# Optimization experiments

Measured on AMD Instinct MI355X. Metric: run time of the kernel, lower is better.

The kernel has to match this reference:

```python
import jax, jax.numpy as jnp
import numpy as np

B, C, D, H, W = 4, 320, 16, 16, 16
E, DK, DV = 2, 32, 160  # heads, key dim, value dim
EPS = 1e-6


def setup_inputs() -> dict:
    key = jax.random.key(0)
    ks = jax.random.split(key, 8)
    s_in = 1.0 / np.sqrt(C)
    s_mg = 1.0 / np.sqrt(E * DV)
    return {
        "x": jax.random.normal(ks[0], (B, C, D, H, W), jnp.float32),
        # pointwise (1x1x1) conv weights, stacked over heads
        "Wq": jax.random.normal(ks[1], (E, DK, C), jnp.float32) * s_in,
        "bq": jax.random.normal(ks[2], (E, DK), jnp.float32) * 0.01,
        "Wk": jax.random.normal(ks[3], (E, DK, C), jnp.float32) * s_in,
        "bk": jax.random.normal(ks[4], (E, DK), jnp.float32) * 0.01,
        "Wv": jax.random.normal(ks[5], (E, DV, C), jnp.float32) * s_in,
        "bv": jax.random.normal(ks[6], (E, DV), jnp.float32) * 0.01,
        # merging 1x1x1 conv: dv*num_heads -> C
        "Wm": jax.random.normal(ks[7], (C, E * DV), jnp.float32) * s_mg,
        "bm": jnp.zeros((C,), jnp.float32),
    }


def reference(x, Wq, bq, Wk, bk, Wv, bv, Wm, bm):
    b, c = x.shape[0], x.shape[1]
    xf = x.reshape(b, c, -1)  # [B, C, N], N = prod(spatial)

    def proj(Wt, bt):
        # 1x1x1 conv over all heads at once: [B, E, d, N]
        return jnp.einsum('ekc,bcn->bekn', Wt, xf) + bt[None, :, :, None]

    Q = proj(Wq, bq)
    K = proj(Wk, bk)
    V = proj(Wv, bv)  # [B, E, DV, N]

    def l2norm(t):
        # F.normalize over channel dim (dim=1 of [B, dk, N] per head)
        n = jnp.linalg.norm(t, axis=2, keepdims=True)
        return t / jnp.maximum(n, EPS)

    Qn = l2norm(Q)
    Kn = l2norm(K)

    # spatial attention: contract over key channels -> [B, E, N, N]
    A = jax.nn.softmax(jnp.einsum('bekn,bekm->benm', Qn, Kn), axis=-1)
    R = jnp.einsum('benm,bevm->bevn', A, V)  # [B, E, DV, N]

    # concat heads along channel dim, then merge conv + residual
    Rcat = R.reshape(b, E * DV, -1)  # [B, E*DV, N]
    out = jnp.einsum('cf,bfn->bcn', Wm, Rcat) + bm[None, :, None]
    return out.reshape(x.shape) + x
```

## Files before the change

### kernel.cpp

```cpp
#include <hip/hip_runtime.h>
#include <hip/hip_bf16.h>

#define BN 4
#define CN 320
#define NN 4096
#define EN 2
#define DKN 32
#define DVN 160

typedef __bf16 bf16;
typedef __bf16 bf16x8 __attribute__((ext_vector_type(8)));
typedef float f32x4 __attribute__((ext_vector_type(4)));

static __device__ __forceinline__ f32x4 mfma16(bf16x8 a, bf16x8 b, f32x4 c) {
  return __builtin_amdgcn_mfma_f32_16x16x32_bf16(a, b, c, 0, 0, 0);
}


__global__ __launch_bounds__(256) void k_prep(
    const float* __restrict__ Wq, const float* __restrict__ bq,
    const float* __restrict__ Wk, const float* __restrict__ bk,
    const float* __restrict__ Wv, const float* __restrict__ bv,
    const float* __restrict__ Wm,
    bf16* __restrict__ W_all, bf16* __restrict__ Wm_bf, float* __restrict__ b_all) {
  int t = blockIdx.x * 256 + threadIdx.x;
  if (t < 448 * CN) {
    int r = t / CN;
    float v;
    if (r < 64) v = Wq[t];
    else if (r < 128) v = Wk[t - 64 * CN];
    else v = Wv[t - 128 * CN];
    W_all[t] = (bf16)v;
  }
  if (t < 320 * 320) Wm_bf[t] = (bf16)Wm[t];
  if (t < 448) {
    float v;
    if (t < 64) v = bq[t];
    else if (t < 128) v = bk[t - 64];
    else v = bv[t - 128];
    b_all[t] = v;
  }
}

__global__ __launch_bounds__(256) void k_xt(const float* __restrict__ x, bf16* __restrict__ xT) {
  int blk = blockIdx.x;
  int b = blk / 640;
  int rem = blk - b * 640;
  int cc = rem >> 4;
  int nb = rem & 15;
  int n = nb * 256 + threadIdx.x;
  const float* xp = x + ((size_t)b * CN + cc * 8) * NN + n;
  bf16x8 v;
#pragma unroll
  for (int j = 0; j < 8; j++) v[j] = (bf16)xp[(size_t)j * NN];
  *(bf16x8*)(xT + ((size_t)b * NN + n) * CN + cc * 8) = v;
}

__global__ __launch_bounds__(256) void k_proj(
    const bf16* __restrict__ W_all, const float* __restrict__ b_all,
    const bf16* __restrict__ xT, float* __restrict__ QK, bf16* __restrict__ Vc) {
  int blk = blockIdx.x;
  int b = blk / 448;
  int rem = blk - b * 448;
  int mt = rem >> 4, nb = rem & 15;
  int w = threadIdx.x >> 6, l = threadIdx.x & 63;
  int lg = l >> 4, lr = l & 15;
  int m0 = mt * 16;
  int n0 = nb * 256 + w * 64;
  f32x4 acc[4] = {};
  const bf16* wp = W_all + (m0 + lr) * CN + 8 * lg;
  const bf16* xp = xT + ((size_t)b * NN + n0 + lr) * CN + 8 * lg;
#pragma unroll 2
  for (int c0 = 0; c0 < CN; c0 += 32) {
    bf16x8 a = *(const bf16x8*)(wp + c0);
#pragma unroll
    for (int j = 0; j < 4; j++) {
      bf16x8 bb = *(const bf16x8*)(xp + j * 16 * CN + c0);
      acc[j] = mfma16(a, bb, acc[j]);
    }
  }
#pragma unroll
  for (int i = 0; i < 4; i++) {
    int row = m0 + 4 * lg + i;
    float bias = b_all[row];
    if (row < 128) {
      float* qk = QK + ((size_t)b * 128 + row) * NN + n0 + lr;
#pragma unroll
      for (int j = 0; j < 4; j++) qk[j * 16] = acc[j][i] + bias;
    } else {
      int rr = row - 128;
      int e = rr / 160, dvl = rr - e * 160;
      int vt = dvl >> 4, lrc = dvl & 15;
      size_t beI = (size_t)(b * 2 + e);
#pragma unroll
      for (int j = 0; j < 4; j++) {
        int key = n0 + j * 16 + lr;
        int T = key >> 5, h = (key >> 4) & 1, g = (key >> 2) & 3, ic = key & 3;
        Vc[(((beI * 128 + T) * 10 + vt) * 4 + g) * 128 + lrc * 8 + h * 4 + ic] =
            (bf16)(acc[j][i] + bias);
      }
    }
  }
}

__global__ __launch_bounds__(256) void k_norm(
    const float* __restrict__ QK, bf16* __restrict__ Qn, bf16* __restrict__ Kn) {
  int t = blockIdx.x * 256 + threadIdx.x;
  int isk = t >> 15;
  int r = t & 32767;
  int b = r >> 13, e = (r >> 12) & 1, n = r & (NN - 1);
  const float* p = QK + ((size_t)b * 128 + isk * 64 + e * 32) * NN + n;
  float v[32];
  float ss = 0.f;
#pragma unroll
  for (int d = 0; d < 32; d++) { float q = p[(size_t)d * NN]; v[d] = q; ss += q * q; }
  float s = 1.0f / fmaxf(sqrtf(ss), 1e-6f);
  bf16* o = (isk ? Kn : Qn) + ((size_t)(b * 2 + e) * NN + n) * 32;
#pragma unroll
  for (int d0 = 0; d0 < 32; d0 += 8) {
    bf16x8 vo;
#pragma unroll
    for (int j = 0; j < 8; j++) vo[j] = (bf16)(v[d0 + j] * s);
    *(bf16x8*)(o + d0) = vo;
  }
}

__global__ __launch_bounds__(256) void k_attn(
    const bf16* __restrict__ Qn, const bf16* __restrict__ Kn,
    const bf16* __restrict__ Vc, bf16* __restrict__ Rt) {
  __shared__ float sbuf[64][83];
  int blk = blockIdx.x;
  int be = blk & 7, qc = blk >> 3;
  int w = threadIdx.x >> 6, l = threadIdx.x & 63;
  int lg = l >> 4, lr = l & 15;
  int qb = qc * 32;
  const bf16* qbase = Qn + ((size_t)be * NN + qb) * 32 + 8 * lg;
  bf16x8 qf0 = *(const bf16x8*)(qbase + lr * 32);
  bf16x8 qf1 = *(const bf16x8*)(qbase + (16 + lr) * 32);
  const bf16* kbase = Kn + (size_t)be * NN * 32 + 8 * lg;
  const bf16* vbase = Vc + (size_t)be * (128 * 10 * 512) + (size_t)l * 8;
  int mstart = w * (NN / 4), mend = mstart + (NN / 4);
  f32x4 acc0[10] = {};
  f32x4 acc1[10] = {};
  float rs0 = 0.f, rs1 = 0.f;
  bf16x8 kf0 = *(const bf16x8*)(kbase + (size_t)(mstart + lr) * 32);
  bf16x8 kf1 = *(const bf16x8*)(kbase + (size_t)(mstart + 16 + lr) * 32);
  for (int m0 = mstart; m0 < mend; m0 += 32) {
    const bf16* vp = vbase + (size_t)(m0 >> 5) * (10 * 512);
    bf16x8 vf[10];
#pragma unroll
    for (int vt = 0; vt < 10; vt++) vf[vt] = *(const bf16x8*)(vp + vt * 512);
    f32x4 zero = {};
    f32x4 s00 = mfma16(kf0, qf0, zero);
    f32x4 s01 = mfma16(kf1, qf0, zero);
    f32x4 s10 = mfma16(kf0, qf1, zero);
    f32x4 s11 = mfma16(kf1, qf1, zero);
    if (m0 + 32 < mend) {
      kf0 = *(const bf16x8*)(kbase + (size_t)(m0 + 32 + lr) * 32);
      kf1 = *(const bf16x8*)(kbase + (size_t)(m0 + 48 + lr) * 32);
    }
    bf16x8 pf0, pf1;
#pragma unroll
    for (int i = 0; i < 4; i++) {
      float e00 = __expf(s00[i]), e01 = __expf(s01[i]);
      float e10 = __expf(s10[i]), e11 = __expf(s11[i]);
      rs0 += e00 + e01;
      rs1 += e10 + e11;
      pf0[i] = (bf16)e00; pf0[4 + i] = (bf16)e01;
      pf1[i] = (bf16)e10; pf1[4 + i] = (bf16)e11;
    }
    __builtin_amdgcn_s_setprio(1);
#pragma unroll
    for (int vt = 0; vt < 10; vt++) {
      acc0[vt] = mfma16(pf0, vf[vt], acc0[vt]);
      acc1[vt] = mfma16(pf1, vf[vt], acc1[vt]);
    }
    __builtin_amdgcn_s_setprio(0);
  }
  for (int r = 1; r < 4; ++r) {
    if (w == r) {
      float* p = &sbuf[l][0];
#pragma unroll
      for (int vt = 0; vt < 10; vt++)
#pragma unroll
        for (int i = 0; i < 4; i++) {
          p[vt * 4 + i] = acc0[vt][i];
          p[40 + vt * 4 + i] = acc1[vt][i];
        }
      p[80] = rs0; p[81] = rs1;
    }
    __syncthreads();
    if (w == 0) {
      const float* p = &sbuf[l][0];
#pragma unroll
      for (int vt = 0; vt < 10; vt++)
#pragma unroll
        for (int i = 0; i < 4; i++) {
          acc0[vt][i] += p[vt * 4 + i];
          acc1[vt][i] += p[40 + vt * 4 + i];
        }
      rs0 += p[80]; rs1 += p[81];
    }
    __syncthreads();
  }
  if (w == 0) {
    rs0 += __shfl_xor(rs0, 16); rs0 += __shfl_xor(rs0, 32);
    rs1 += __shfl_xor(rs1, 16); rs1 += __shfl_xor(rs1, 32);
    f32x4 rinv0, rinv1;
#pragma unroll
    for (int i = 0; i < 4; i++) {
      rinv0[i] = 1.0f / __shfl(rs0, 4 * lg + i);
      rinv1[i] = 1.0f / __shfl(rs1, 4 * lg + i);
    }
    int b = be >> 1, e = be & 1;
#pragma unroll
    for (int vt = 0; vt < 10; vt++) {
#pragma unroll
      for (int i = 0; i < 4; i++) {
        int q0 = qb + 4 * lg + i;
        int q1 = qb + 16 + 4 * lg + i;
        Rt[((size_t)b * NN + q0) * 320 + e * 160 + vt * 16 + lr] = (bf16)(acc0[vt][i] * rinv0[i]);
        Rt[((size_t)b * NN + q1) * 320 + e * 160 + vt * 16 + lr] = (bf16)(acc1[vt][i] * rinv1[i]);
      }
    }
  }
}

__global__ __launch_bounds__(256) void k_merge(
    const bf16* __restrict__ Wm_bf, const float* __restrict__ bm,
    const bf16* __restrict__ Rt, const float* __restrict__ x, float* __restrict__ out) {
  int blk = blockIdx.x;
  int b = blk / 320;
  int rem = blk - b * 320;
  int ct = rem >> 4, nb = rem & 15;
  int w = threadIdx.x >> 6, l = threadIdx.x & 63;
  int lg = l >> 4, lr = l & 15;
  int c0 = ct * 16, n0 = nb * 256 + w * 64;
  f32x4 acc[4] = {};
  const bf16* ap = Wm_bf + (c0 + lr) * 320 + 8 * lg;
  const bf16* bp = Rt + ((size_t)b * NN + n0 + lr) * 320 + 8 * lg;
#pragma unroll 2
  for (int f0 = 0; f0 < 320; f0 += 32) {
    bf16x8 a = *(const bf16x8*)(ap + f0);
#pragma unroll
    for (int j = 0; j < 4; j++) {
      bf16x8 bb = *(const bf16x8*)(bp + j * 16 * 320 + f0);
      acc[j] = mfma16(a, bb, acc[j]);
    }
  }
#pragma unroll
  for (int i = 0; i < 4; i++) {
    int c = c0 + 4 * lg + i;
    float bias = bm[c];
    const float* xp = x + ((size_t)b * 320 + c) * NN + n0 + lr;
    float* op = out + ((size_t)b * 320 + c) * NN + n0 + lr;
#pragma unroll
    for (int j = 0; j < 4; j++) op[j * 16] = acc[j][i] + bias + xp[j * 16];
  }
}

extern "C" void kernel_launch(void* const* d_in, const int* in_sizes, int n_in,
                              void* d_out, int out_size, void* d_ws, size_t ws_size,
                              hipStream_t stream) {
  const float* x  = (const float*)d_in[0];
  const float* Wq = (const float*)d_in[1];
  const float* bq = (const float*)d_in[2];
  const float* Wk = (const float*)d_in[3];
  const float* bk = (const float*)d_in[4];
  const float* Wv = (const float*)d_in[5];
  const float* bv = (const float*)d_in[6];
  const float* Wm = (const float*)d_in[7];
  const float* bm = (const float*)d_in[8];
  float* out = (float*)d_out;
  char* ws = (char*)d_ws;
  bf16*  W_all = (bf16*)(ws + 0);
  bf16*  Wm_bf = (bf16*)(ws + 286720);
  float* b_all = (float*)(ws + 491520);
  bf16*  xT    = (bf16*)(ws + 493568);
  float* QK    = (float*)(ws + 10979328);
  bf16*  Qn    = (bf16*)(ws + 19367936);
  bf16*  Kn    = (bf16*)(ws + 21465088);
  bf16*  Vc    = (bf16*)(ws + 23562240);
  bf16*  Rt    = (bf16*)(ws + 34048000);

  k_prep<<<560, 256, 0, stream>>>(Wq, bq, Wk, bk, Wv, bv, Wm, W_all, Wm_bf, b_all);
  k_xt<<<2560, 256, 0, stream>>>(x, xT);
  k_proj<<<1792, 256, 0, stream>>>(W_all, b_all, xT, QK, Vc);
  k_norm<<<256, 256, 0, stream>>>(QK, Qn, Kn);
  k_attn<<<1024, 256, 0, stream>>>(Qn, Kn, Vc, Rt);
  k_merge<<<1280, 256, 0, stream>>>(Wm_bf, bm, Rt, x, out);
}
```

Measured before the change: 236.4 us.

## Split attention queries across waves instead of keys, double-buffer K/V loads

Each wave now owns its own 32 queries and scans the full key range, so the shared-memory cross-wave reduction of accumulators and row sums disappears. The grid shrinks from 1024 to 256 blocks, and K/V fragments are loaded with explicit A/B double buffering plus a periodic block barrier to keep the waves in step for cache reuse. Launch bounds pin one block per SIMD group, trading fewer resident blocks and a long serial key loop per wave for no reduction overhead and better prefetching.

```diff
diff --git a/kernel.cpp b/kernel.cpp
--- a/kernel.cpp
+++ b/kernel.cpp
@@ -125,103 +125,92 @@
   }
 }
 
-__global__ __launch_bounds__(256) void k_attn(
+__global__ __launch_bounds__(256, 1) void k_attn(
     const bf16* __restrict__ Qn, const bf16* __restrict__ Kn,
     const bf16* __restrict__ Vc, bf16* __restrict__ Rt) {
-  __shared__ float sbuf[64][83];
   int blk = blockIdx.x;
   int be = blk & 7, qc = blk >> 3;
   int w = threadIdx.x >> 6, l = threadIdx.x & 63;
   int lg = l >> 4, lr = l & 15;
-  int qb = qc * 32;
+  int qb = qc * 128 + w * 32;
   const bf16* qbase = Qn + ((size_t)be * NN + qb) * 32 + 8 * lg;
   bf16x8 qf0 = *(const bf16x8*)(qbase + lr * 32);
   bf16x8 qf1 = *(const bf16x8*)(qbase + (16 + lr) * 32);
   const bf16* kbase = Kn + (size_t)be * NN * 32 + 8 * lg;
-  const bf16* vbase = Vc + (size_t)be * (128 * 10 * 512) + (size_t)l * 8;
-  int mstart = w * (NN / 4), mend = mstart + (NN / 4);
+  const bf16* vbase = Vc + (size_t)be * (128 * 5120) + (size_t)l * 8;
   f32x4 acc0[10] = {};
   f32x4 acc1[10] = {};
   float rs0 = 0.f, rs1 = 0.f;
-  bf16x8 kf0 = *(const bf16x8*)(kbase + (size_t)(mstart + lr) * 32);
-  bf16x8 kf1 = *(const bf16x8*)(kbase + (size_t)(mstart + 16 + lr) * 32);
-  for (int m0 = mstart; m0 < mend; m0 += 32) {
-    const bf16* vp = vbase + (size_t)(m0 >> 5) * (10 * 512);
-    bf16x8 vf[10];
-#pragma unroll
-    for (int vt = 0; vt < 10; vt++) vf[vt] = *(const bf16x8*)(vp + vt * 512);
-    f32x4 zero = {};
-    f32x4 s00 = mfma16(kf0, qf0, zero);
-    f32x4 s01 = mfma16(kf1, qf0, zero);
-    f32x4 s10 = mfma16(kf0, qf1, zero);
-    f32x4 s11 = mfma16(kf1, qf1, zero);
-    if (m0 + 32 < mend) {
-      kf0 = *(const bf16x8*)(kbase + (size_t)(m0 + 32 + lr) * 32);
-      kf1 = *(const bf16x8*)(kbase + (size_t)(m0 + 48 + lr) * 32);
-    }
-    bf16x8 pf0, pf1;
+  bf16x8 kfA0 = *(const bf16x8*)(kbase + (size_t)lr * 32);
+  bf16x8 kfA1 = *(const bf16x8*)(kbase + (size_t)(16 + lr) * 32);
+  bf16x8 vA[10], vB[10], kfB0, kfB1;
+#pragma unroll
+  for (int vt = 0; vt < 10; vt++) vA[vt] = *(const bf16x8*)(vbase + vt * 512);
+
+#define PROCESS(KF0, KF1, VF)                                              \
+  {                                                                        \
+    f32x4 zero = {};                                                       \
+    f32x4 s00 = mfma16(KF0, qf0, zero);                                    \
+    f32x4 s01 = mfma16(KF1, qf0, zero);                                    \
+    f32x4 s10 = mfma16(KF0, qf1, zero);                                    \
+    f32x4 s11 = mfma16(KF1, qf1, zero);                                    \
+    bf16x8 pf0, pf1;                                                       \
+    _Pragma("unroll") for (int i = 0; i < 4; i++) {                        \
+      float e00 = __expf(s00[i]), e01 = __expf(s01[i]);                    \
+      float e10 = __expf(s10[i]), e11 = __expf(s11[i]);                    \
+      rs0 += e00 + e01;                                                    \
+      rs1 += e10 + e11;                                                    \
+      pf0[i] = (bf16)e00; pf0[4 + i] = (bf16)e01;                          \
+      pf1[i] = (bf16)e10; pf1[4 + i] = (bf16)e11;                          \
+    }                                                                      \
+    __builtin_amdgcn_s_setprio(1);                                         \
+    _Pragma("unroll") for (int vt = 0; vt < 10; vt++) {                    \
+      acc0[vt] = mfma16(pf0, VF[vt], acc0[vt]);                            \
+      acc1[vt] = mfma16(pf1, VF[vt], acc1[vt]);                            \
+    }                                                                      \
+    __builtin_amdgcn_s_setprio(0);                                         \
+  }
+
+  for (int T = 0; T < 128; T += 2) {
+    {
+      const bf16* kp = kbase + (size_t)((T + 1) * 32 + lr) * 32;
+      kfB0 = *(const bf16x8*)(kp);
+      kfB1 = *(const bf16x8*)(kp + 16 * 32);
+      const bf16* vp = vbase + (size_t)(T + 1) * 5120;
+#pragma unroll
+      for (int vt = 0; vt < 10; vt++) vB[vt] = *(const bf16x8*)(vp + vt * 512);
+    }
+    PROCESS(kfA0, kfA1, vA);
+    if (T + 2 < 128) {
+      const bf16* kp = kbase + (size_t)((T + 2) * 32 + lr) * 32;
+      kfA0 = *(const bf16x8*)(kp);
+      kfA1 = *(const bf16x8*)(kp + 16 * 32);
+      const bf16* vp = vbase + (size_t)(T + 2) * 5120;
+#pragma unroll
+      for (int vt = 0; vt < 10; vt++) vA[vt] = *(const bf16x8*)(vp + vt * 512);
+    }
+    PROCESS(kfB0, kfB1, vB);
+    if ((T & 6) == 6) __syncthreads();
+  }
+#undef PROCESS
+
+  rs0 += __shfl_xor(rs0, 16); rs0 += __shfl_xor(rs0, 32);
+  rs1 += __shfl_xor(rs1, 16); rs1 += __shfl_xor(rs1, 32);
+  f32x4 rinv0, rinv1;
+#pragma unroll
+  for (int i = 0; i < 4; i++) {
+    rinv0[i] = 1.0f / __shfl(rs0, 4 * lg + i);
+    rinv1[i] = 1.0f / __shfl(rs1, 4 * lg + i);
+  }
+  int b = be >> 1, e = be & 1;
+#pragma unroll
+  for (int vt = 0; vt < 10; vt++) {
 #pragma unroll
     for (int i = 0; i < 4; i++) {
-      float e00 = __expf(s00[i]), e01 = __expf(s01[i]);
-      float e10 = __expf(s10[i]), e11 = __expf(s11[i]);
-      rs0 += e00 + e01;
-      rs1 += e10 + e11;
-      pf0[i] = (bf16)e00; pf0[4 + i] = (bf16)e01;
-      pf1[i] = (bf16)e10; pf1[4 + i] = (bf16)e11;
-    }
-    __builtin_amdgcn_s_setprio(1);
-#pragma unroll
-    for (int vt = 0; vt < 10; vt++) {
-      acc0[vt] = mfma16(pf0, vf[vt], acc0[vt]);
-      acc1[vt] = mfma16(pf1, vf[vt], acc1[vt]);
-    }
-    __builtin_amdgcn_s_setprio(0);
-  }
-  for (int r = 1; r < 4; ++r) {
-    if (w == r) {
-      float* p = &sbuf[l][0];
-#pragma unroll
-      for (int vt = 0; vt < 10; vt++)
-#pragma unroll
-        for (int i = 0; i < 4; i++) {
-          p[vt * 4 + i] = acc0[vt][i];
-          p[40 + vt * 4 + i] = acc1[vt][i];
-        }
-      p[80] = rs0; p[81] = rs1;
-    }
-    __syncthreads();
-    if (w == 0) {
-      const float* p = &sbuf[l][0];
-#pragma unroll
-      for (int vt = 0; vt < 10; vt++)
-#pragma unroll
-        for (int i = 0; i < 4; i++) {
-          acc0[vt][i] += p[vt * 4 + i];
-          acc1[vt][i] += p[40 + vt * 4 + i];
-        }
-      rs0 += p[80]; rs1 += p[81];
-    }
-    __syncthreads();
-  }
-  if (w == 0) {
-    rs0 += __shfl_xor(rs0, 16); rs0 += __shfl_xor(rs0, 32);
-    rs1 += __shfl_xor(rs1, 16); rs1 += __shfl_xor(rs1, 32);
-    f32x4 rinv0, rinv1;
-#pragma unroll
-    for (int i = 0; i < 4; i++) {
-      rinv0[i] = 1.0f / __shfl(rs0, 4 * lg + i);
-      rinv1[i] = 1.0f / __shfl(rs1, 4 * lg + i);
-    }
-    int b = be >> 1, e = be & 1;
-#pragma unroll
-    for (int vt = 0; vt < 10; vt++) {
-#pragma unroll
-      for (int i = 0; i < 4; i++) {
-        int q0 = qb + 4 * lg + i;
-        int q1 = qb + 16 + 4 * lg + i;
-        Rt[((size_t)b * NN + q0) * 320 + e * 160 + vt * 16 + lr] = (bf16)(acc0[vt][i] * rinv0[i]);
-        Rt[((size_t)b * NN + q1) * 320 + e * 160 + vt * 16 + lr] = (bf16)(acc1[vt][i] * rinv1[i]);
-      }
+      int q0 = qb + 4 * lg + i;
+      int q1 = qb + 16 + 4 * lg + i;
+      Rt[((size_t)b * NN + q0) * 320 + e * 160 + vt * 16 + lr] = (bf16)(acc0[vt][i] * rinv0[i]);
+      Rt[((size_t)b * NN + q1) * 320 + e * 160 + vt * 16 + lr] = (bf16)(acc1[vt][i] * rinv1[i]);
     }
   }
 }
@@ -287,6 +276,6 @@
   k_xt<<<2560, 256, 0, stream>>>(x, xT);
   k_proj<<<1792, 256, 0, stream>>>(W_all, b_all, xT, QK, Vc);
   k_norm<<<256, 256, 0, stream>>>(QK, Qn, Kn);
-  k_attn<<<1024, 256, 0, stream>>>(Qn, Kn, Vc, Rt);
+  k_attn<<<256, 256, 0, stream>>>(Qn, Kn, Vc, Rt);
   k_merge<<<1280, 256, 0, stream>>>(Wm_bf, bm, Rt, x, out);
 }
```

Result: slower. 274.7 us (+16.2%).
